# Performance work log

Measured on AMD Instinct MI355X. Metric: run time of the kernel, lower is better.

## Reference

```python
import jax, jax.numpy as jnp
import numpy as np

T, B, E = 2048, 2, 1024
H, R = 16, 8
HD = E // H          # head_dim = 64
VD = E // R          # value_dim = attn_dim // num_rules = 128 (attn_dim = embed_dim)
SEL = E // H         # selection_dim = 64


def _linear_params(key, out_dim, in_dim):
    kw, kb = jax.random.split(key)
    lim = float(np.sqrt(6.0 / (in_dim + out_dim)))  # xavier_uniform
    W = jax.random.uniform(kw, (out_dim, in_dim), jnp.float32, -lim, lim)
    b = jnp.zeros((out_dim,), jnp.float32)
    return W, b


def setup_inputs() -> dict:
    key = jax.random.key(0)
    ks = jax.random.split(key, 7)
    query = jax.random.normal(ks[0], (T, B, E), jnp.float32)
    Wq, bq = _linear_params(ks[1], E, E)
    Wk, bk = _linear_params(ks[2], E, E)
    Wv, bv = _linear_params(ks[3], E, E)          # v_proj: embed_dim -> attn_dim (=E)
    Wvq, bvq = _linear_params(ks[4], SEL * H, E)  # value_q (q_compose=False)
    Wsc, bsc = _linear_params(ks[5], 1, SEL + VD) # score_network (nonlinear=False)
    Wo, bo = _linear_params(ks[6], E, H * VD)     # out_proj
    return {"query": query, "Wq": Wq, "bq": bq, "Wk": Wk, "bk": bk,
            "Wv": Wv, "bv": bv, "Wvq": Wvq, "bvq": bvq,
            "Wsc": Wsc, "bsc": bsc, "Wo": Wo, "bo": bo}


def reference(query, Wq, bq, Wk, bk, Wv, bv, Wvq, bvq, Wsc, bsc, Wo, bo):
    t, b, e = query.shape
    scaling = HD ** -0.5
    # projections (self-attention: k, v from query)
    q = (query @ Wq.T + bq) * scaling                       # (T,B,E)
    k = query @ Wk.T + bk                                   # (T,B,E)
    v = query @ Wv.T + bv                                   # (T,B,attn_dim)
    q = q.reshape(t, b, H, HD).transpose(1, 2, 0, 3)        # (B,H,T,HD)
    k = k.reshape(t, b, H, HD).transpose(1, 2, 0, 3)        # (B,H,S,HD)
    v = v.reshape(t, b, R, VD).transpose(1, 2, 0, 3)        # (B,R,S,VD)
    # standard multi-head search: softmax over source positions
    probs = jax.nn.softmax(jnp.einsum('bhtd,bhsd->bhts', q, k), axis=-1)
    # per-(head, rule) retrieved values
    attn = jnp.einsum('bhts,brsd->bhtrd', probs, v)         # (B,H,T,R,VD)
    # selection query from raw input (q_compose=False)
    v_q = (query @ Wvq.T + bvq).reshape(t, b, H, SEL).transpose(1, 2, 0, 3)  # (B,H,T,SEL)
    v_q = jnp.broadcast_to(v_q[:, :, :, None, :], (b, H, t, R, SEL))
    comp = jnp.concatenate([v_q, attn], axis=-1)            # (B,H,T,R,SEL+VD)
    score = comp @ Wsc.T + bsc                              # (B,H,T,R,1)
    sel = jax.nn.softmax(score, axis=3)                     # softmax over rules
    out = jnp.sum(attn * sel, axis=3)                       # (B,H,T,VD)
    out = out.transpose(2, 0, 1, 3).reshape(t, b, H * VD)   # (T,B,H*VD)
    return out @ Wo.T + bo                                  # (T,B,E)
```

## Files before the change

kernel.cpp:

```cpp
#include <hip/hip_runtime.h>
#include <hip/hip_bf16.h>
#include <stdint.h>

typedef unsigned short u16;
typedef unsigned int u32;
typedef __attribute__((ext_vector_type(8))) short bf16x8;
typedef __attribute__((ext_vector_type(4))) float f32x4;

#define TT 2048
#define BB 2
#define HH 16
#define RR 8
#define SS 2048
#define MROWS 4096

__device__ __forceinline__ float bf2f(u16 h){ union { u32 u; float f; } v; v.u = ((u32)h) << 16; return v.f; }
__device__ __forceinline__ u16 f2bf(float f){ union { float f; u32 u; } v; v.f = f; return (u16)((v.u + 0x7FFFu + ((v.u >> 16) & 1u)) >> 16); }
__device__ __forceinline__ void gl_lds16(const void* g, void* l){
  __builtin_amdgcn_global_load_lds((const __attribute__((address_space(1))) u32*)g,
                                   (__attribute__((address_space(3))) u32*)l, 16, 0, 0);
}

__global__ void k_cvt(const float* __restrict__ s, u16* __restrict__ d, int n, float scale){
  int i = blockIdx.x * blockDim.x + threadIdx.x;
  int st = gridDim.x * blockDim.x;
  for (; i < n; i += st) d[i] = f2bf(s[i] * scale);
}

__global__ void k_bias(const float* __restrict__ bq, const float* __restrict__ bk,
                       const float* __restrict__ bv, float* __restrict__ bb){
  int i = blockIdx.x * blockDim.x + threadIdx.x;
  if (i < 1024){ bb[i] = bq[i] * 0.125f; bb[1024 + i] = bk[i]; bb[2048 + i] = bv[i]; }
}

template<int KD, bool OBF>
__launch_bounds__(256, 2)
__global__ void k_gemm(const u16* __restrict__ A, const u16* __restrict__ Bt,
                       const float* __restrict__ bias, void* __restrict__ Cout, int ldc){
  __shared__ u16 As[128*32];
  __shared__ u16 Bs[128*32];
  const int tid = threadIdx.x, lane = tid & 63, wid = tid >> 6;
  const int mw = wid >> 1, nw = wid & 1;
  const int m0 = blockIdx.y * 128, n0 = blockIdx.x * 128;
  const f32x4 fzero = {0.f, 0.f, 0.f, 0.f};
  f32x4 acc[4][4];
  #pragma unroll
  for (int a = 0; a < 4; ++a)
    #pragma unroll
    for (int c = 0; c < 4; ++c) acc[a][c] = fzero;

  for (int k0 = 0; k0 < KD; k0 += 32){
    #pragma unroll
    for (int it = 0; it < 2; ++it){
      int c = it*256 + tid, r = c >> 2, sl = c & 3;
      gl_lds16(A + (size_t)(m0 + r)*KD + k0 + 8*(sl ^ ((r >> 1) & 3)), &As[c*8]);
    }
    #pragma unroll
    for (int it = 0; it < 2; ++it){
      int c = it*256 + tid, r = c >> 2, sl = c & 3;
      gl_lds16(Bt + (size_t)(n0 + r)*KD + k0 + 8*(sl ^ ((r >> 1) & 3)), &Bs[c*8]);
    }
    __syncthreads();
    bf16x8 af[4], bfr[4];
    #pragma unroll
    for (int mt = 0; mt < 4; ++mt){
      int r = mw*64 + mt*16 + (lane & 15);
      int pos = (lane >> 4) ^ ((r >> 1) & 3);
      af[mt] = *(const bf16x8*)&As[r*32 + pos*8];
    }
    #pragma unroll
    for (int nt = 0; nt < 4; ++nt){
      int r = nw*64 + nt*16 + (lane & 15);
      int pos = (lane >> 4) ^ ((r >> 1) & 3);
      bfr[nt] = *(const bf16x8*)&Bs[r*32 + pos*8];
    }
    #pragma unroll
    for (int mt = 0; mt < 4; ++mt)
      #pragma unroll
      for (int nt = 0; nt < 4; ++nt)
        acc[mt][nt] = __builtin_amdgcn_mfma_f32_16x16x32_bf16(af[mt], bfr[nt], acc[mt][nt], 0, 0, 0);
    __syncthreads();
  }
  #pragma unroll
  for (int nt = 0; nt < 4; ++nt){
    int col = n0 + nw*64 + nt*16 + (lane & 15);
    float bvv = bias[col];
    #pragma unroll
    for (int mt = 0; mt < 4; ++mt)
      #pragma unroll
      for (int j = 0; j < 4; ++j){
        int row = m0 + mw*64 + mt*16 + (lane >> 4)*4 + j;
        float v = acc[mt][nt][j] + bvv;
        if constexpr (OBF) ((u16*)Cout)[(size_t)row*ldc + col] = f2bf(v);
        else               ((float*)Cout)[(size_t)row*ldc + col] = v;
      }
  }
}

__global__ void k_transpose(const u16* __restrict__ qkvb, u16* __restrict__ Vt2){
  __shared__ u16 tile[32][33];
  const int b = blockIdx.z;
  const int s0 = blockIdx.x * 32, n0 = blockIdx.y * 32;
  const int tx = threadIdx.x & 31, ty = threadIdx.x >> 5;
  for (int i = ty; i < 32; i += 8)
    tile[i][tx] = qkvb[(size_t)((s0 + i)*BB + b)*3072 + 2048 + n0 + tx];
  __syncthreads();
  for (int i = ty; i < 32; i += 8){
    int c = n0 + i;
    int nr = ((c & 127) << 3) | (c >> 7);
    Vt2[(size_t)b*1024*SS + (size_t)nr*SS + s0 + tx] = tile[tx][i];
  }
}

__global__ void k_vw2(const u16* __restrict__ qkvb, const float* __restrict__ Wsc,
                      u16* __restrict__ vwa){
  int idx = blockIdx.x * blockDim.x + threadIdx.x;
  if (idx >= BB*16*SS) return;
  int s = idx & (SS - 1);
  int r = (idx >> 11) & 15;
  int b = idx >> 15;
  float a;
  if (r < 8){
    const u16* vrow = qkvb + (size_t)(s*BB + b)*3072 + 2048 + r*128;
    a = 0.f;
    #pragma unroll 8
    for (int d = 0; d < 128; ++d) a += bf2f(vrow[d]) * Wsc[64 + d];
  } else if (r == 8) a = 1.0f;
  else a = 0.f;
  vwa[(size_t)(b*16 + r)*SS + s] = f2bf(a);
}

__launch_bounds__(512, 4)
__global__ void k_attn2(const u16* __restrict__ qkvb, const u16* __restrict__ vwa,
                        u16* __restrict__ probs, float* __restrict__ selp, int bh0){
  __shared__ u16 Qs[64*64];
  __shared__ u16 Ks[128*64];
  __shared__ u16 P[64*136];
  __shared__ float pwL[8][16][16];
  const int tid = threadIdx.x, lane = tid & 63, wid = tid >> 6;
  const int bhl = blockIdx.y;
  const int bh = bh0 + bhl;
  const int t0 = blockIdx.x * 64;
  const int b = bh >> 4, h = bh & 15;
  const u16* qbase = qkvb + b*3072 + h*64;
  const u16* kbase = qkvb + b*3072 + 1024 + h*64;
  const u16* vwbase = vwa + (size_t)b*16*SS;
  u16* pbase = probs + ((size_t)bhl*TT + t0)*SS;
  const f32x4 fzero = {0.f, 0.f, 0.f, 0.f};

  {
    int c = tid, r = c >> 3, sl = c & 7;
    gl_lds16(qbase + (size_t)(t0 + r)*6144 + 8*(sl ^ (r & 7)), &Qs[c*8]);
  }
  __syncthreads();
  bf16x8 qf[4][2];
  #pragma unroll
  for (int mt = 0; mt < 4; ++mt)
    #pragma unroll
    for (int kk = 0; kk < 2; ++kk){
      int r = mt*16 + (lane & 15);
      int pos = (kk*4 + (lane >> 4)) ^ (r & 7);
      qf[mt][kk] = *(const bf16x8*)&Qs[r*64 + pos*8];
    }

  f32x4 pwacc = fzero;
  const int mtp = wid & 3, kks = (wid >> 2)*2;

  for (int s0 = 0; s0 < SS; s0 += 128){
    #pragma unroll
    for (int it = 0; it < 2; ++it){
      int c = it*512 + tid, r = c >> 3, sl = c & 7;
      gl_lds16(kbase + (size_t)(s0 + r)*6144 + 8*(sl ^ (r & 7)), &Ks[c*8]);
    }
    __syncthreads();
    bf16x8 kf[2];
    #pragma unroll
    for (int kk = 0; kk < 2; ++kk){
      int r = wid*16 + (lane & 15);
      int pos = (kk*4 + (lane >> 4)) ^ (r & 7);
      kf[kk] = *(const bf16x8*)&Ks[r*64 + pos*8];
    }
    #pragma unroll
    for (int bt = 0; bt < 4; ++bt){
      f32x4 sa = fzero;
      sa = __builtin_amdgcn_mfma_f32_16x16x32_bf16(kf[0], qf[bt][0], sa, 0, 0, 0);
      sa = __builtin_amdgcn_mfma_f32_16x16x32_bf16(kf[1], qf[bt][1], sa, 0, 0, 0);
      u32 w0 = (u32)f2bf(__expf(sa[0])) | ((u32)f2bf(__expf(sa[1])) << 16);
      u32 w1 = (u32)f2bf(__expf(sa[2])) | ((u32)f2bf(__expf(sa[3])) << 16);
      int t = bt*16 + (lane & 15);
      int sl = wid*16 + (lane >> 4)*4;
      uint2 pk; pk.x = w0; pk.y = w1;
      *(uint2*)&P[t*136 + sl] = pk;
    }
    __syncthreads();
    bf16x8 vwf[2];
    #pragma unroll
    for (int kq = 0; kq < 2; ++kq)
      vwf[kq] = *(const bf16x8*)&vwbase[(size_t)(lane & 15)*SS + s0 + (kks + kq)*32 + (lane >> 4)*8];
    #pragma unroll
    for (int kq = 0; kq < 2; ++kq){
      int kk = kks + kq;
      bf16x8 pa = *(const bf16x8*)&P[(mtp*16 + (lane & 15))*136 + kk*32 + (lane >> 4)*8];
      pwacc = __builtin_amdgcn_mfma_f32_16x16x32_bf16(pa, vwf[kq], pwacc, 0, 0, 0);
    }
    #pragma unroll
    for (int cc = 0; cc < 2; ++cc){
      int c = cc*512 + tid;
      int row = c >> 4, col = c & 15;
      bf16x8 v = *(const bf16x8*)&P[row*136 + col*8];
      *(bf16x8*)&pbase[(size_t)row*SS + s0 + col*8] = v;
    }
  }

  #pragma unroll
  for (int j = 0; j < 4; ++j)
    pwL[wid][(lane >> 4)*4 + j][lane & 15] = pwacc[j];
  __syncthreads();
  if (tid < 64){
    int mt = tid >> 4, tr = tid & 15;
    float pw[9];
    #pragma unroll
    for (int r = 0; r < 9; ++r) pw[r] = pwL[mt][tr][r] + pwL[mt + 4][tr][r];
    float rs = pw[8];
    float inv = 1.0f / rs;
    float mx = -3.0e38f;
    #pragma unroll
    for (int r = 0; r < 8; ++r) mx = fmaxf(mx, pw[r]*inv);
    float e[8], ssum = 0.f;
    #pragma unroll
    for (int r = 0; r < 8; ++r){ e[r] = __expf(pw[r]*inv - mx); ssum += e[r]; }
    #pragma unroll
    for (int r = 0; r < 8; ++r)
      selp[((size_t)bh*TT + t0 + tid)*8 + r] = e[r] / (ssum * rs);
  }
}

__launch_bounds__(512, 2)
__global__ void k_pv4(const u16* __restrict__ probs, const u16* __restrict__ Vt2,
                      const float* __restrict__ selp, u16* __restrict__ oattn,
                      int bh0, int G){
  __shared__ u16 L[4*16384];
  const int tid = threadIdx.x, lane = tid & 63, wid = tid >> 6;
  const int mw = wid & 1, nw2 = wid >> 1;
  int fid = blockIdx.x, bhl, xy;
  if (G >= 8){ bhl = (fid & 7) + 8*(fid >> 8); xy = (fid >> 3) & 31; }
  else       { bhl = fid >> 5;                 xy = fid & 31; }
  const int t0 = (xy >> 2) * 256;
  const int n0 = (xy & 3) * 256;
  const int bh = bh0 + bhl, b = bh >> 4, h = bh & 15;
  const u16* Abase = probs + ((size_t)bhl*TT + t0)*SS;
  const u16* Bbase = Vt2 + (size_t)b*1024*SS + (size_t)n0*SS;
  const f32x4 fzero = {0.f, 0.f, 0.f, 0.f};
  f32x4 acc[8][4];
  #pragma unroll
  for (int a = 0; a < 8; ++a)
    #pragma unroll
    for (int c = 0; c < 4; ++c) acc[a][c] = fzero;

  auto stage = [&](int q){
    u16* As = &L[(q & 3) * 16384];
    u16* Bs = As + 8192;
    #pragma unroll
    for (int i = 0; i < 2; ++i){
      int ci = i*512 + tid, r = ci >> 2, sl = ci & 3;
      gl_lds16(Abase + (size_t)r*SS + q*32 + 8*(sl ^ ((r >> 1) & 3)), &As[ci*8]);
    }
    #pragma unroll
    for (int i = 0; i < 2; ++i){
      int ci = i*512 + tid, r = ci >> 2, sl = ci & 3;
      gl_lds16(Bbase + (size_t)r*SS + q*32 + 8*(sl ^ ((r >> 1) & 3)), &Bs[ci*8]);
    }
  };

  stage(0); stage(1); stage(2);
  asm volatile("s_waitcnt vmcnt(8)" ::: "memory");
  __builtin_amdgcn_s_barrier();
  __builtin_amdgcn_sched_barrier(0);

  for (int q = 0; q < 64; ++q){
    const u16* As = &L[(q & 3) * 16384];
    const u16* Bs = As + 8192;
    bf16x8 af[8], bfr[4];
    #pragma unroll
    for (int mf = 0; mf < 8; ++mf){
      int r = mw*128 + mf*16 + (lane & 15);
      int pos = (lane >> 4) ^ ((r >> 1) & 3);
      af[mf] = *(const bf16x8*)&As[r*32 + pos*8];
    }
    #pragma unroll
    for (int nf = 0; nf < 4; ++nf){
      int r = nw2*64 + nf*16 + (lane & 15);
      int pos = (lane >> 4) ^ ((r >> 1) & 3);
      bfr[nf] = *(const bf16x8*)&Bs[r*32 + pos*8];
    }
    if (q + 3 < 64) stage(q + 3);
    __builtin_amdgcn_s_setprio(1);
    #pragma unroll
    for (int mf = 0; mf < 8; ++mf)
      #pragma unroll
      for (int nf = 0; nf < 4; ++nf)
        acc[mf][nf] = __builtin_amdgcn_mfma_f32_16x16x32_bf16(af[mf], bfr[nf], acc[mf][nf], 0, 0, 0);
    __builtin_amdgcn_s_setprio(0);
    if (q < 61)       asm volatile("s_waitcnt vmcnt(8)" ::: "memory");
    else if (q == 61) asm volatile("s_waitcnt vmcnt(4)" ::: "memory");
    else              asm volatile("s_waitcnt vmcnt(0)" ::: "memory");
    __builtin_amdgcn_s_barrier();
    __builtin_amdgcn_sched_barrier(0);
  }

  const int c15 = lane & 15, g = lane >> 4, r8 = c15 & 7;
  float sel[8][4];
  #pragma unroll
  for (int mf = 0; mf < 8; ++mf)
    #pragma unroll
    for (int j = 0; j < 4; ++j){
      int trow = t0 + mw*128 + mf*16 + g*4 + j;
      sel[mf][j] = selp[((size_t)bh*TT + trow)*8 + r8];
    }
  #pragma unroll
  for (int mf = 0; mf < 8; ++mf)
    #pragma unroll
    for (int nf = 0; nf < 4; ++nf){
      float v0 = acc[mf][nf][0] * sel[mf][0];
      float v1 = acc[mf][nf][1] * sel[mf][1];
      float v2 = acc[mf][nf][2] * sel[mf][2];
      float v3 = acc[mf][nf][3] * sel[mf][3];
      #pragma unroll
      for (int mask = 1; mask < 8; mask <<= 1){
        v0 += __shfl_xor(v0, mask, 64);
        v1 += __shfl_xor(v1, mask, 64);
        v2 += __shfl_xor(v2, mask, 64);
        v3 += __shfl_xor(v3, mask, 64);
      }
      if (r8 == 0){
        int dglob = (n0 >> 3) + nw2*8 + nf*2 + (c15 >> 3);
        int tb = t0 + mw*128 + mf*16 + g*4;
        u16* dst = oattn + (size_t)(tb*BB + b)*2048 + h*128 + dglob;
        dst[0*BB*2048] = f2bf(v0);
        dst[1*BB*2048] = f2bf(v1);
        dst[2*BB*2048] = f2bf(v2);
        dst[3*BB*2048] = f2bf(v3);
      }
    }
}

extern "C" void kernel_launch(void* const* d_in, const int* in_sizes, int n_in,
                              void* d_out, int out_size, void* d_ws, size_t ws_size,
                              hipStream_t stream){
  (void)in_sizes; (void)n_in;
  const float* query = (const float*)d_in[0];
  const float* Wq  = (const float*)d_in[1];
  const float* bq  = (const float*)d_in[2];
  const float* Wk  = (const float*)d_in[3];
  const float* bk  = (const float*)d_in[4];
  const float* Wv  = (const float*)d_in[5];
  const float* bv  = (const float*)d_in[6];
  const float* Wsc = (const float*)d_in[9];
  const float* Wo  = (const float*)d_in[11];
  const float* bo  = (const float*)d_in[12];

  char* p = (char*)d_ws;
  auto carve = [&](size_t bytes) -> char* {
    char* r = p; p += (bytes + 255) & ~((size_t)255); return r;
  };
  u16*   Xb     = (u16*)  carve((size_t)MROWS*1024*2);
  u16*   Wb     = (u16*)  carve((size_t)3072*1024*2);
  u16*   Wob    = (u16*)  carve((size_t)1024*2048*2);
  float* bb     = (float*)carve(3072*4);
  u16*   qkvb   = (u16*)  carve((size_t)MROWS*3072*2);
  u16*   Vt2    = (u16*)  carve((size_t)BB*1024*SS*2);
  u16*   vwa    = (u16*)  carve((size_t)BB*16*SS*2);
  u16*   oattn  = (u16*)  carve((size_t)MROWS*2048*2);
  float* selp   = (float*)carve((size_t)32*TT*RR*4);
  size_t fixed = (size_t)(p - (char*)d_ws);
  int G = 32;
  while (G > 1 && fixed + ((size_t)G*TT*SS*2 + 256) > ws_size) G >>= 1;
  u16* probs;
  if (fixed + ((size_t)G*TT*SS*2 + 256) <= ws_size){
    probs = (u16*)carve((size_t)G*TT*SS*2);
  } else {
    G = 1;
    probs = Xb;
  }

  k_cvt<<<1024, 256, 0, stream>>>(query, Xb, MROWS*1024, 1.0f);
  k_cvt<<<512, 256, 0, stream>>>(Wq, Wb, 1024*1024, 0.125f);
  k_cvt<<<512, 256, 0, stream>>>(Wk, Wb + 1024*1024, 1024*1024, 1.0f);
  k_cvt<<<512, 256, 0, stream>>>(Wv, Wb + 2*1024*1024, 1024*1024, 1.0f);
  k_cvt<<<1024, 256, 0, stream>>>(Wo, Wob, 1024*2048, 1.0f);
  k_bias<<<4, 256, 0, stream>>>(bq, bk, bv, bb);
  k_gemm<1024, true><<<dim3(24, 32), 256, 0, stream>>>(Xb, Wb, bb, qkvb, 3072);
  k_transpose<<<dim3(64, 32, 2), 256, 0, stream>>>(qkvb, Vt2);
  k_vw2<<<256, 256, 0, stream>>>(qkvb, Wsc, vwa);
  for (int bh0 = 0; bh0 < 32; bh0 += G){
    k_attn2<<<dim3(32, G), 512, 0, stream>>>(qkvb, vwa, probs, selp, bh0);
    k_pv4<<<G*32, 512, 0, stream>>>(probs, Vt2, selp, oattn, bh0, G);
  }
  k_gemm<2048, false><<<dim3(8, 32), 256, 0, stream>>>(oattn, Wob, bo, d_out, 1024);
}
```

Baseline: 433.5 us.

## Shrink PV GEMM block to 128x256 tile with 4 waves and triple buffering

The probs×V GEMM block tile shrinks from 256x256 with 8 waves to 128x256 with 4 waves. Each wave now owns the full 128 rows of the M dimension, and the number of blocks doubles. The LDS pipeline goes from 4 slots with prefetch depth 3 to 3 slots with prefetch depth 2, which cuts LDS use per block and may let more blocks fit per CU. The cost is that each block reloads the V tile for half as many rows, so global traffic for V goes up and latency hiding is shallower.

Result: slower. 459.3 us (+6.0%).

```diff
diff --git a/kernel.cpp b/kernel.cpp
--- a/kernel.cpp
+++ b/kernel.cpp
@@ -235,17 +235,16 @@
   }
 }
 
-__launch_bounds__(512, 2)
-__global__ void k_pv4(const u16* __restrict__ probs, const u16* __restrict__ Vt2,
+__launch_bounds__(256, 2)
+__global__ void k_pv9(const u16* __restrict__ probs, const u16* __restrict__ Vt2,
                       const float* __restrict__ selp, u16* __restrict__ oattn,
                       int bh0, int G){
-  __shared__ u16 L[4*16384];
-  const int tid = threadIdx.x, lane = tid & 63, wid = tid >> 6;
-  const int mw = wid & 1, nw2 = wid >> 1;
+  __shared__ u16 L[3*12288];
+  const int tid = threadIdx.x, lane = tid & 63, w = tid >> 6;
   int fid = blockIdx.x, bhl, xy;
-  if (G >= 8){ bhl = (fid & 7) + 8*(fid >> 8); xy = (fid >> 3) & 31; }
-  else       { bhl = fid >> 5;                 xy = fid & 31; }
-  const int t0 = (xy >> 2) * 256;
+  if (G >= 8){ bhl = (fid & 7) + 8*(fid >> 9); xy = (fid >> 3) & 63; }
+  else       { bhl = fid >> 6;                 xy = fid & 63; }
+  const int t0 = (xy >> 2) * 128;
   const int n0 = (xy & 3) * 256;
   const int bh = bh0 + bhl, b = bh >> 4, h = bh & 15;
   const u16* Abase = probs + ((size_t)bhl*TT + t0)*SS;
@@ -257,43 +256,44 @@
     #pragma unroll
     for (int c = 0; c < 4; ++c) acc[a][c] = fzero;
 
-  auto stage = [&](int q){
-    u16* As = &L[(q & 3) * 16384];
-    u16* Bs = As + 8192;
+  auto stage = [&](int q, int slot){
+    u16* As = &L[slot * 12288];
+    u16* Bs = As + 4096;
     #pragma unroll
     for (int i = 0; i < 2; ++i){
-      int ci = i*512 + tid, r = ci >> 2, sl = ci & 3;
+      int ci = i*256 + tid, r = ci >> 2, sl = ci & 3;
       gl_lds16(Abase + (size_t)r*SS + q*32 + 8*(sl ^ ((r >> 1) & 3)), &As[ci*8]);
     }
     #pragma unroll
-    for (int i = 0; i < 2; ++i){
-      int ci = i*512 + tid, r = ci >> 2, sl = ci & 3;
+    for (int i = 0; i < 4; ++i){
+      int ci = i*256 + tid, r = ci >> 2, sl = ci & 3;
       gl_lds16(Bbase + (size_t)r*SS + q*32 + 8*(sl ^ ((r >> 1) & 3)), &Bs[ci*8]);
     }
   };
 
-  stage(0); stage(1); stage(2);
-  asm volatile("s_waitcnt vmcnt(8)" ::: "memory");
+  stage(0, 0); stage(1, 1);
+  asm volatile("s_waitcnt vmcnt(6)" ::: "memory");
   __builtin_amdgcn_s_barrier();
   __builtin_amdgcn_sched_barrier(0);
 
+  int cs = 0, ss = 2;
   for (int q = 0; q < 64; ++q){
-    const u16* As = &L[(q & 3) * 16384];
-    const u16* Bs = As + 8192;
+    const u16* As = &L[cs * 12288];
+    const u16* Bs = As + 4096;
     bf16x8 af[8], bfr[4];
     #pragma unroll
     for (int mf = 0; mf < 8; ++mf){
-      int r = mw*128 + mf*16 + (lane & 15);
+      int r = mf*16 + (lane & 15);
       int pos = (lane >> 4) ^ ((r >> 1) & 3);
       af[mf] = *(const bf16x8*)&As[r*32 + pos*8];
     }
     #pragma unroll
     for (int nf = 0; nf < 4; ++nf){
-      int r = nw2*64 + nf*16 + (lane & 15);
+      int r = w*64 + nf*16 + (lane & 15);
       int pos = (lane >> 4) ^ ((r >> 1) & 3);
       bfr[nf] = *(const bf16x8*)&Bs[r*32 + pos*8];
     }
-    if (q + 3 < 64) stage(q + 3);
+    if (q + 2 < 64) stage(q + 2, ss);
     __builtin_amdgcn_s_setprio(1);
     #pragma unroll
     for (int mf = 0; mf < 8; ++mf)
@@ -301,11 +301,12 @@
       for (int nf = 0; nf < 4; ++nf)
         acc[mf][nf] = __builtin_amdgcn_mfma_f32_16x16x32_bf16(af[mf], bfr[nf], acc[mf][nf], 0, 0, 0);
     __builtin_amdgcn_s_setprio(0);
-    if (q < 61)       asm volatile("s_waitcnt vmcnt(8)" ::: "memory");
-    else if (q == 61) asm volatile("s_waitcnt vmcnt(4)" ::: "memory");
-    else              asm volatile("s_waitcnt vmcnt(0)" ::: "memory");
+    if (q < 62) asm volatile("s_waitcnt vmcnt(6)" ::: "memory");
+    else        asm volatile("s_waitcnt vmcnt(0)" ::: "memory");
     __builtin_amdgcn_s_barrier();
     __builtin_amdgcn_sched_barrier(0);
+    cs = (cs == 2) ? 0 : cs + 1;
+    ss = (ss == 2) ? 0 : ss + 1;
   }
 
   const int c15 = lane & 15, g = lane >> 4, r8 = c15 & 7;
@@ -314,7 +315,7 @@
   for (int mf = 0; mf < 8; ++mf)
     #pragma unroll
     for (int j = 0; j < 4; ++j){
-      int trow = t0 + mw*128 + mf*16 + g*4 + j;
+      int trow = t0 + mf*16 + g*4 + j;
       sel[mf][j] = selp[((size_t)bh*TT + trow)*8 + r8];
     }
   #pragma unroll
@@ -333,8 +334,8 @@
         v3 += __shfl_xor(v3, mask, 64);
       }
       if (r8 == 0){
-        int dglob = (n0 >> 3) + nw2*8 + nf*2 + (c15 >> 3);
-        int tb = t0 + mw*128 + mf*16 + g*4;
+        int dglob = (n0 >> 3) + w*8 + nf*2 + (c15 >> 3);
+        int tb = t0 + mf*16 + g*4;
         u16* dst = oattn + (size_t)(tb*BB + b)*2048 + h*128 + dglob;
         dst[0*BB*2048] = f2bf(v0);
         dst[1*BB*2048] = f2bf(v1);
@@ -394,7 +395,7 @@
   k_vw2<<<256, 256, 0, stream>>>(qkvb, Wsc, vwa);
   for (int bh0 = 0; bh0 < 32; bh0 += G){
     k_attn2<<<dim3(32, G), 512, 0, stream>>>(qkvb, vwa, probs, selp, bh0);
-    k_pv4<<<G*32, 512, 0, stream>>>(probs, Vt2, selp, oattn, bh0, G);
+    k_pv9<<<G*64, 256, 0, stream>>>(probs, Vt2, selp, oattn, bh0, G);
   }
   k_gemm<2048, false><<<dim3(8, 32), 256, 0, stream>>>(oattn, Wob, bo, d_out, 1024);
 }
```
